# Performance work log

Hardware: AMD Instinct MI355X
Metric: run time of the kernel (lower is better)

Reference implementation:

```python
import jax, jax.numpy as jnp
import numpy as np

# config matching init_kwargs
J = 5
Q = 8
T = 15
C = 4
J_PHI = 2
B = 4
N = 65536

# near_sym_b level-1 lowpass (13-tap) from the dtcwt library; highpass via QMF modulation.
H0O = np.array([-0.00455690456024, -0.00543947593727, 0.01702522388155, 0.02382538479492,
                -0.10671180468666, 0.01186609203379, 0.56881042071212, 0.75614564389252,
                0.27529538466888, -0.11720388769911, -0.03887280126882, 0.03466034684485,
                -0.00388321199915], dtype=np.float32)
H1O = (((-1.0) ** np.arange(13)) * H0O[::-1]).astype(np.float32)
# qshift_a 10-tap filters for levels >= 2 (tree b = time-reversed tree a)
H0A = np.array([0.03516384, 0.0, -0.08832942, 0.23389032, 0.76027237,
                0.58751830, 0.0, -0.11430184, 0.0, 0.0], dtype=np.float32)
H0B = H0A[::-1].copy()
H1A = (((-1.0) ** np.arange(10)) * H0B).astype(np.float32)
H1B = H1A[::-1].copy()


def _dwconv(x, h, dilation):
    # depthwise 'same' conv; x: (B,C,N), h: (K,) fixed wavelet filter
    c = x.shape[1]
    k = h.shape[0]
    w = jnp.tile(jnp.asarray(h, x.dtype)[None, None, :], (c, 1, 1))
    tot = dilation * (k - 1)
    return jax.lax.conv_general_dilated(
        x, w, (1,), [(tot // 2, tot - tot // 2)], rhs_dilation=(dilation,),
        dimension_numbers=("NCH", "OIH", "NCH"), feature_group_count=c)


def _gconv(x, w, dilation):
    # grouped learnable conv: x (B,C,N), w (Q*C,1,T), groups=C, 'same' padding
    c = x.shape[1]
    t = w.shape[-1]
    tot = dilation * (t - 1)
    return jax.lax.conv_general_dilated(
        x, w, (1,), [(tot // 2, tot - tot // 2)], rhs_dilation=(dilation,),
        dimension_numbers=("NCH", "OIH", "NCH"), feature_group_count=c)


def _udtcwt(x):
    # undecimated dual-tree CWT (a-trous): returns lowpass and J (real, imag) bandpass pairs
    la, lb = x, x
    bps = []
    for j in range(J):
        d = 1 if j == 0 else 2 ** (j - 1)
        if j == 0:
            h0a, h1a, h0b, h1b = H0O, H1O, H0O, H1O
        else:
            h0a, h1a, h0b, h1b = H0A, H1A, H0B, H1B
        bps.append((_dwconv(la, h1a, d), _dwconv(lb, h1b, d)))
        la = _dwconv(la, h0a, d)
        lb = _dwconv(lb, h0b, d)
    return 0.5 * (la + lb), bps


def _downsample(x):
    # J_phi x (near_sym_b lowpass then ::2 decimation)
    for _ in range(J_PHI):
        x = _dwconv(x, H0O, 1)[:, :, ::2]
    return x


def _forward(x, conv_w, roots, beta):
    lp, bps = _udtcwt(x)
    outs = []
    for j in range(J):
        d = 1 if j == 0 else 2 ** (j - 1)
        scale = 2.0 ** (0.5 * j)  # sqrt(2)**j
        r = _gconv(bps[j][0], conv_w[j], d) / scale
        im = _gconv(bps[j][1], conv_w[j], d) / scale
        u = jnp.sqrt(r * r + im * im)  # ModulusStable
        alpha = jax.nn.sigmoid(roots[j])[None, :, None]  # (1, Q*C, 1)
        u = (jnp.maximum(u, -beta) + beta) ** alpha  # PowerStable
        outs.append(_downsample(u))
    return jnp.concatenate(outs, axis=1)  # (B, C*J*Q, N/2**J_phi)


def setup_inputs() -> dict:
    key = jax.random.key(0)
    kx, kw = jax.random.split(key)
    x = jax.random.normal(kx, (B, C, N), dtype=jnp.float32)
    bound = float(1.0 / np.sqrt(T))  # torch Conv1d default init (in/groups=1)
    conv_w = jax.random.uniform(kw, (J, Q * C, 1, T), dtype=jnp.float32, minval=-bound, maxval=bound)
    roots = jnp.ones((J, Q * C), dtype=jnp.float32)  # module inits root to ones
    beta = jnp.full((1,), 0.01, dtype=jnp.float32)
    return {"x": x, "conv_w": conv_w, "roots": roots, "beta": beta}


def reference(x, conv_w, roots, beta):
    return _forward(x, conv_w, roots, beta)
```

## Files before the change

### kernel.cpp

```cpp
#include <hip/hip_runtime.h>
#include <hip/hip_bf16.h>

typedef float v2f __attribute__((ext_vector_type(2)));

#define B_    4
#define C_    4
#define Q_    8
#define J_    5
#define T_    15
#define NSIG  65536
#define N2SIG 32768
#define NOUT  16384
#define NCH   (B_ * C_)

constexpr float H0Oc[13] = {
    -0.00455690456024f, -0.00543947593727f,  0.01702522388155f,  0.02382538479492f,
    -0.10671180468666f,  0.01186609203379f,  0.56881042071212f,  0.75614564389252f,
     0.27529538466888f, -0.11720388769911f, -0.03887280126882f,  0.03466034684485f,
    -0.00388321199915f };
constexpr float H1Oc[13] = {
    -0.00388321199915f, -0.03466034684485f, -0.03887280126882f,  0.11720388769911f,
     0.27529538466888f, -0.75614564389252f,  0.56881042071212f, -0.01186609203379f,
    -0.10671180468666f, -0.02382538479492f,  0.01702522388155f,  0.00543947593727f,
    -0.00455690456024f };
constexpr float H0Ac[10] = {
     0.03516384f, 0.0f, -0.08832942f, 0.23389032f, 0.76027237f,
     0.58751830f, 0.0f, -0.11430184f, 0.0f, 0.0f };
constexpr float H0Bc[10] = {
     0.0f, 0.0f, -0.11430184f, 0.0f, 0.58751830f,
     0.76027237f, 0.23389032f, -0.08832942f, 0.0f, 0.03516384f };
constexpr float H1Ac[10] = {
     0.0f, 0.0f, -0.11430184f, 0.0f, 0.58751830f,
    -0.76027237f, 0.23389032f, 0.08832942f, 0.0f, -0.03516384f };
constexpr float H1Bc[10] = {
    -0.03516384f, 0.0f, 0.08832942f, 0.23389032f, -0.76027237f,
     0.58751830f, 0.0f, -0.11430184f, 0.0f, 0.0f };

struct Gtab { float v[37]; };
constexpr Gtab make_g() {
    Gtab g{};
    for (int n = 0; n < 37; ++n) {
        float s = 0.f;
        for (int k = 0; k < 13; ++k) {
            int l = n - 2 * k;
            if (l >= 0 && l < 13) s += H0Oc[k] * H0Oc[l];
        }
        g.v[n] = s;
    }
    return g;
}
constexpr Gtab cG = make_g();

#define M2    256
#define NUcnt 1057
#define NUP   1064
#define NBcnt 1169
#define NBP   1176
#define S_    1320

#define SMEM_FLOATS (5280 + 2 * NBP)

__device__ __forceinline__ v2f zmask(v2f a, bool ok) {
    if (!ok) { a.x = 0.f; a.y = 0.f; }
    return a;
}

template<int D, bool EDGE>
__device__ __forceinline__ void post_stage(
        const v2f* __restrict__ sRI, v2f* __restrict__ U0, v2f* __restrict__ U1,
        const float* __restrict__ cw, const float* __restrict__ roots,
        float beta, int j, int b, int c, int m0, int mt, int tid,
        float* __restrict__ out) {
    const float lg_is = -0.5f * (float)j;
    const float beta2 = beta * exp2f(0.5f * (float)j);
    const int   u_lo  = 4 * m0 - 18;

    for (int g2 = 0; g2 < 2; ++g2) {
        float w[4][T_], al[4], cq[4];
        #pragma unroll
        for (int qq = 0; qq < 4; ++qq) {
            const int o = c * Q_ + g2 * 4 + qq;
            #pragma unroll
            for (int t = 0; t < T_; t++) w[qq][t] = cw[(size_t)(j * 32 + o) * T_ + t];
            al[qq] = 1.f / (1.f + __expf(-roots[j * 32 + o]));
            cq[qq] = al[qq] * lg_is;
        }

        for (int i = tid; i < NUcnt; i += 256) {
            const v2f* tp = sRI + (i + 56 - 7 * D);
            v2f taps[T_];
            #pragma unroll
            for (int t = 0; t < T_; t++) taps[t] = tp[t * D];
            bool ok = true;
            if constexpr (EDGE) {
                const int n = u_lo + i;
                ok = ((unsigned)n < (unsigned)NSIG);
            }
            float uq[4];
            #pragma unroll
            for (int qq = 0; qq < 4; ++qq) {
                v2f ri; ri.x = 0.f; ri.y = 0.f;
                #pragma unroll
                for (int t = 0; t < T_; t++) ri += w[qq][t] * taps[t];
                float z2 = fmaf(ri.x, ri.x, ri.y * ri.y);
                float us = __builtin_amdgcn_sqrtf(z2);
                float lg = __builtin_amdgcn_logf(us + beta2);
                float u  = __builtin_amdgcn_exp2f(fmaf(al[qq], lg, cq[qq]));
                if constexpr (EDGE) uq[qq] = ok ? u : 0.f;
                else                uq[qq] = u;
            }
            v2f p0; p0.x = uq[0]; p0.y = uq[1];
            v2f p1; p1.x = uq[2]; p1.y = uq[3];
            U0[i] = p0; U1[i] = p1;
        }
        __syncthreads();

        {
            const int m = m0 + tid;
            #pragma unroll
            for (int qp = 0; qp < 2; ++qp) {
                const v2f* up = qp ? U1 : U0;
                const v2f* ub = up + 4 * tid;
                v2f acc; acc.x = 0.f; acc.y = 0.f;
                #pragma unroll
                for (int n = 0; n < 37; ++n) acc += cG.v[n] * ub[n];
                if constexpr (EDGE) {
                    const bool edge = (mt == 0 && tid < 3) || (mt == 63 && tid >= 253);
                    if (edge) {
                        v2f a2; a2.x = 0.f; a2.y = 0.f;
                        for (int k = 0; k < 13; ++k) {
                            int p = 2 * m + k - 6;
                            if (p < 0 || p >= N2SIG) continue;
                            v2f v; v.x = 0.f; v.y = 0.f;
                            for (int l = 0; l < 13; ++l)
                                v += H0Oc[l] * up[4 * tid + 2 * k + l];
                            a2 += H0Oc[k] * v;
                        }
                        acc = a2;
                    }
                }
                const int o = c * Q_ + g2 * 4 + 2 * qp;
                out[((size_t)b * 160 + j * 32 + o)     * NOUT + m] = acc.x;
                out[((size_t)b * 160 + j * 32 + o + 1) * NOUT + m] = acc.y;
            }
        }
        __syncthreads();
    }
}

template<bool EDGE>
__device__ __forceinline__ void run_tile(
        float* __restrict__ smem,
        const float* __restrict__ x, const float* __restrict__ cw,
        const float* __restrict__ roots, float beta,
        float* __restrict__ out, int j, int mt, int ch, int tid) {
    float* X   = smem;
    float* L1  = smem + S_;
    v2f*   PP0 = (v2f*)smem;
    v2f*   PP1 = (v2f*)(smem + 2 * S_);
    v2f*   U0  = (v2f*)smem;
    v2f*   U1  = (v2f*)(smem + 2 * NUP);
    v2f*   sRI = (v2f*)(smem + 4 * S_);

    const int b   = ch >> 2, c = ch & 3;
    const int m0  = mt * M2;
    const int ofs = 4 * m0 - 147;
    const float* xc = x + (size_t)ch * NSIG;

    for (int p = tid; p < S_; p += 256) {
        if constexpr (EDGE) {
            int g = ofs + p;
            X[p] = ((unsigned)g < (unsigned)NSIG) ? xc[g] : 0.f;
        } else {
            X[p] = xc[ofs + p];
        }
    }
    __syncthreads();

    if (j == 0) {
        for (int i = tid; i < NBcnt; i += 256) {
            int p = 73 + i;
            float a = 0.f;
            #pragma unroll
            for (int k = 0; k < 13; k++) a += H1Oc[k] * X[p + k - 6];
            if constexpr (EDGE) { if ((unsigned)(ofs + p) >= (unsigned)NSIG) a = 0.f; }
            v2f r; r.x = a; r.y = a;
            sRI[i] = r;
        }
    } else {
        for (int p = 6 + tid; p < 1313; p += 256) {
            float a = 0.f;
            #pragma unroll
            for (int k = 0; k < 13; k++) a += H0Oc[k] * X[p + k - 6];
            if constexpr (EDGE) { if ((unsigned)(ofs + p) >= (unsigned)NSIG) a = 0.f; }
            L1[p] = a;
        }
        __syncthreads();
        if (j == 1) {
            for (int i = tid; i < NBcnt; i += 256) {
                int p = 73 + i;
                v2f r; r.x = 0.f; r.y = 0.f;
                #pragma unroll
                for (int k = 0; k < 10; k++) {
                    v2f hk; hk.x = H1Ac[k]; hk.y = H1Bc[k];
                    r += hk * L1[p + k - 4];
                }
                if constexpr (EDGE) r = zmask(r, (unsigned)(ofs + p) < (unsigned)NSIG);
                sRI[i] = r;
            }
        } else {
            for (int p = 10 + tid; p < 1308; p += 256) {
                v2f a; a.x = 0.f; a.y = 0.f;
                #pragma unroll
                for (int k = 0; k < 10; k++) {
                    v2f hk; hk.x = H0Ac[k]; hk.y = H0Bc[k];
                    a += hk * L1[p + k - 4];
                }
                if constexpr (EDGE) a = zmask(a, (unsigned)(ofs + p) < (unsigned)NSIG);
                PP1[p] = a;
            }
            __syncthreads();
            if (j == 2) {
                for (int i = tid; i < NBcnt; i += 256) {
                    int p = 73 + i;
                    v2f r; r.x = 0.f; r.y = 0.f;
                    #pragma unroll
                    for (int k = 0; k < 10; k++) {
                        v2f hk; hk.x = H1Ac[k]; hk.y = H1Bc[k];
                        r += hk * PP1[p + 2 * k - 9];
                    }
                    if constexpr (EDGE) r = zmask(r, (unsigned)(ofs + p) < (unsigned)NSIG);
                    sRI[i] = r;
                }
            } else {
                for (int p = 19 + tid; p < 1299; p += 256) {
                    v2f a; a.x = 0.f; a.y = 0.f;
                    #pragma unroll
                    for (int k = 0; k < 10; k++) {
                        v2f hk; hk.x = H0Ac[k]; hk.y = H0Bc[k];
                        a += hk * PP1[p + 2 * k - 9];
                    }
                    if constexpr (EDGE) a = zmask(a, (unsigned)(ofs + p) < (unsigned)NSIG);
                    PP0[p] = a;
                }
                __syncthreads();
                if (j == 3) {
                    for (int i = tid; i < NBcnt; i += 256) {
                        int p = 73 + i;
                        v2f r; r.x = 0.f; r.y = 0.f;
                        #pragma unroll
                        for (int k = 0; k < 10; k++) {
                            v2f hk; hk.x = H1Ac[k]; hk.y = H1Bc[k];
                            r += hk * PP0[p + 4 * k - 18];
                        }
                        if constexpr (EDGE) r = zmask(r, (unsigned)(ofs + p) < (unsigned)NSIG);
                        sRI[i] = r;
                    }
                } else {
                    for (int p = 37 + tid; p < 1281; p += 256) {
                        v2f a; a.x = 0.f; a.y = 0.f;
                        #pragma unroll
                        for (int k = 0; k < 10; k++) {
                            v2f hk; hk.x = H0Ac[k]; hk.y = H0Bc[k];
                            a += hk * PP0[p + 4 * k - 18];
                        }
                        if constexpr (EDGE) a = zmask(a, (unsigned)(ofs + p) < (unsigned)NSIG);
                        PP1[p] = a;
                    }
                    __syncthreads();
                    for (int i = tid; i < NBcnt; i += 256) {
                        int p = 73 + i;
                        v2f r; r.x = 0.f; r.y = 0.f;
                        #pragma unroll
                        for (int k = 0; k < 10; k++) {
                            v2f hk; hk.x = H1Ac[k]; hk.y = H1Bc[k];
                            r += hk * PP1[p + 8 * k - 36];
                        }
                        if constexpr (EDGE) r = zmask(r, (unsigned)(ofs + p) < (unsigned)NSIG);
                        sRI[i] = r;
                    }
                }
            }
        }
    }
    __syncthreads();

    float beta_ = beta;
    if (j == 0)      post_stage<1, EDGE>(sRI, U0, U1, cw, roots, beta_, 0, b, c, m0, mt, tid, out);
    else if (j == 1) post_stage<1, EDGE>(sRI, U0, U1, cw, roots, beta_, 1, b, c, m0, mt, tid, out);
    else if (j == 2) post_stage<2, EDGE>(sRI, U0, U1, cw, roots, beta_, 2, b, c, m0, mt, tid, out);
    else if (j == 3) post_stage<4, EDGE>(sRI, U0, U1, cw, roots, beta_, 3, b, c, m0, mt, tid, out);
    else             post_stage<8, EDGE>(sRI, U0, U1, cw, roots, beta_, 4, b, c, m0, mt, tid, out);
}

__global__ __launch_bounds__(256, 5) void murenn_all(
        const float* __restrict__ x,
        const float* __restrict__ cw,
        const float* __restrict__ roots,
        const float* __restrict__ beta_p,
        float* __restrict__ out) {
    __shared__ __align__(16) float smem[SMEM_FLOATS];
    const int tid = threadIdx.x;
    const int mt  = blockIdx.x;
    const int ch  = blockIdx.y;
    const int j   = blockIdx.z;
    const float beta = beta_p[0];

    if (mt == 0 || mt == 63)
        run_tile<true >(smem, x, cw, roots, beta, out, j, mt, ch, tid);
    else
        run_tile<false>(smem, x, cw, roots, beta, out, j, mt, ch, tid);
}

extern "C" void kernel_launch(void* const* d_in, const int* in_sizes, int n_in,
                              void* d_out, int out_size, void* d_ws, size_t ws_size,
                              hipStream_t stream) {
    (void)in_sizes; (void)n_in; (void)out_size; (void)d_ws; (void)ws_size;
    const float* x     = (const float*)d_in[0];
    const float* cw    = (const float*)d_in[1];
    const float* roots = (const float*)d_in[2];
    const float* beta  = (const float*)d_in[3];
    float* out = (float*)d_out;

    dim3 grid(NOUT / M2, NCH, J_);
    murenn_all<<<grid, 256, 0, stream>>>(x, cw, roots, beta, out);
}
```

Baseline: 162.3 us.

## Split fused kernel into shared wavelet-chain pass and per-level post pass via workspace

The fused kernel recomputed the whole undecimated DTCWT filter chain inside every (tile, channel, level) block, so the lower levels were recomputed up to five times. The change adds a chain kernel that computes all five bandpass planes once per tile and channel and writes them as interleaved real/imag pairs to the workspace. A second kernel then loads the plane for its level and runs the existing post stage. This trades the redundant compute for about 42 MB of global write plus read traffic and an extra launch, and it falls back to the fused kernel when no workspace is given.

New measurement: 167.5 us. +3.2%, slower.

```diff
diff --git a/kernel.cpp b/kernel.cpp
--- a/kernel.cpp
+++ b/kernel.cpp
@@ -58,7 +58,12 @@
 #define NBP   1176
 #define S_    1320
 
-#define SMEM_FLOATS (5280 + 2 * NBP)
+#define SMEM_ALL   (5280 + 2 * NBP)
+#define SMEM_CHAIN (4 * S_)
+#define SMEM_POST  (NBP + 2 * NUP)
+
+#define PLANE_V2F  ((size_t)J_ * NCH * NSIG)
+#define WS_BYTES   (PLANE_V2F * sizeof(v2f))
 
 __device__ __forceinline__ v2f zmask(v2f a, bool ok) {
     if (!ok) { a.x = 0.f; a.y = 0.f; }
@@ -145,6 +150,199 @@
             }
         }
         __syncthreads();
+    }
+}
+
+template<bool EDGE>
+__device__ __forceinline__ void chain_tile(
+        float* __restrict__ smem, const float* __restrict__ x,
+        v2f* __restrict__ bp, int mt, int ch, int tid) {
+    float* X   = smem;
+    float* L1  = smem + S_;
+    v2f*   PP0 = (v2f*)smem;
+    v2f*   PP1 = (v2f*)(smem + 2 * S_);
+
+    const int m0  = mt * M2;
+    const int ofs = 4 * m0 - 147;
+    const float* xc = x + (size_t)ch * NSIG;
+
+    for (int p = tid; p < S_; p += 256) {
+        if constexpr (EDGE) {
+            int g = ofs + p;
+            X[p] = ((unsigned)g < (unsigned)NSIG) ? xc[g] : 0.f;
+        } else {
+            X[p] = xc[ofs + p];
+        }
+    }
+    __syncthreads();
+
+    {
+        v2f* dst = bp + (size_t)(0 * NCH + ch) * NSIG + 4 * m0;
+        for (int idx = tid; idx < 1024; idx += 256) {
+            int p = 147 + idx;
+            float a = 0.f;
+            #pragma unroll
+            for (int k = 0; k < 13; k++) a += H1Oc[k] * X[p + k - 6];
+            v2f r; r.x = a; r.y = a;
+            dst[idx] = r;
+        }
+    }
+    for (int p = 6 + tid; p < 1313; p += 256) {
+        float a = 0.f;
+        #pragma unroll
+        for (int k = 0; k < 13; k++) a += H0Oc[k] * X[p + k - 6];
+        if constexpr (EDGE) { if ((unsigned)(ofs + p) >= (unsigned)NSIG) a = 0.f; }
+        L1[p] = a;
+    }
+    __syncthreads();
+
+    {
+        v2f* dst = bp + (size_t)(1 * NCH + ch) * NSIG + 4 * m0;
+        for (int idx = tid; idx < 1024; idx += 256) {
+            int p = 147 + idx;
+            v2f r; r.x = 0.f; r.y = 0.f;
+            #pragma unroll
+            for (int k = 0; k < 10; k++) {
+                v2f hk; hk.x = H1Ac[k]; hk.y = H1Bc[k];
+                r += hk * L1[p + k - 4];
+            }
+            dst[idx] = r;
+        }
+    }
+    for (int p = 10 + tid; p < 1308; p += 256) {
+        v2f a; a.x = 0.f; a.y = 0.f;
+        #pragma unroll
+        for (int k = 0; k < 10; k++) {
+            v2f hk; hk.x = H0Ac[k]; hk.y = H0Bc[k];
+            a += hk * L1[p + k - 4];
+        }
+        if constexpr (EDGE) a = zmask(a, (unsigned)(ofs + p) < (unsigned)NSIG);
+        PP1[p] = a;
+    }
+    __syncthreads();
+
+    {
+        v2f* dst = bp + (size_t)(2 * NCH + ch) * NSIG + 4 * m0;
+        for (int idx = tid; idx < 1024; idx += 256) {
+            int p = 147 + idx;
+            v2f r; r.x = 0.f; r.y = 0.f;
+            #pragma unroll
+            for (int k = 0; k < 10; k++) {
+                v2f hk; hk.x = H1Ac[k]; hk.y = H1Bc[k];
+                r += hk * PP1[p + 2 * k - 9];
+            }
+            dst[idx] = r;
+        }
+    }
+    for (int p = 19 + tid; p < 1299; p += 256) {
+        v2f a; a.x = 0.f; a.y = 0.f;
+        #pragma unroll
+        for (int k = 0; k < 10; k++) {
+            v2f hk; hk.x = H0Ac[k]; hk.y = H0Bc[k];
+            a += hk * PP1[p + 2 * k - 9];
+        }
+        if constexpr (EDGE) a = zmask(a, (unsigned)(ofs + p) < (unsigned)NSIG);
+        PP0[p] = a;
+    }
+    __syncthreads();
+
+    {
+        v2f* dst = bp + (size_t)(3 * NCH + ch) * NSIG + 4 * m0;
+        for (int idx = tid; idx < 1024; idx += 256) {
+            int p = 147 + idx;
+            v2f r; r.x = 0.f; r.y = 0.f;
+            #pragma unroll
+            for (int k = 0; k < 10; k++) {
+                v2f hk; hk.x = H1Ac[k]; hk.y = H1Bc[k];
+                r += hk * PP0[p + 4 * k - 18];
+            }
+            dst[idx] = r;
+        }
+    }
+    for (int p = 37 + tid; p < 1281; p += 256) {
+        v2f a; a.x = 0.f; a.y = 0.f;
+        #pragma unroll
+        for (int k = 0; k < 10; k++) {
+            v2f hk; hk.x = H0Ac[k]; hk.y = H0Bc[k];
+            a += hk * PP0[p + 4 * k - 18];
+        }
+        if constexpr (EDGE) a = zmask(a, (unsigned)(ofs + p) < (unsigned)NSIG);
+        PP1[p] = a;
+    }
+    __syncthreads();
+
+    {
+        v2f* dst = bp + (size_t)(4 * NCH + ch) * NSIG + 4 * m0;
+        for (int idx = tid; idx < 1024; idx += 256) {
+            int p = 147 + idx;
+            v2f r; r.x = 0.f; r.y = 0.f;
+            #pragma unroll
+            for (int k = 0; k < 10; k++) {
+                v2f hk; hk.x = H1Ac[k]; hk.y = H1Bc[k];
+                r += hk * PP1[p + 8 * k - 36];
+            }
+            dst[idx] = r;
+        }
+    }
+}
+
+__global__ __launch_bounds__(256, 5) void murenn_chain(
+        const float* __restrict__ x, v2f* __restrict__ bp) {
+    __shared__ __align__(16) float smem[SMEM_CHAIN];
+    const int tid = threadIdx.x;
+    const int mt  = blockIdx.x;
+    const int ch  = blockIdx.y;
+    if (mt == 0 || mt == 63) chain_tile<true >(smem, x, bp, mt, ch, tid);
+    else                     chain_tile<false>(smem, x, bp, mt, ch, tid);
+}
+
+__global__ __launch_bounds__(256, 6) void murenn_post(
+        const v2f* __restrict__ bp,
+        const float* __restrict__ cw,
+        const float* __restrict__ roots,
+        const float* __restrict__ beta_p,
+        float* __restrict__ out) {
+    __shared__ __align__(16) v2f smemv[SMEM_POST];
+    v2f* sRI = smemv;
+    v2f* U0  = smemv + NBP;
+    v2f* U1  = smemv + NBP + NUP;
+
+    const int tid = threadIdx.x;
+    const int mt  = blockIdx.x;
+    const int ch  = blockIdx.y;
+    const int j   = blockIdx.z;
+    const int b   = ch >> 2, c = ch & 3;
+    const int m0  = mt * M2;
+    const int base = 4 * m0 - 74;
+    const float beta = beta_p[0];
+    const v2f* plane = bp + (size_t)(j * NCH + ch) * NSIG;
+
+    const bool EDGE_T = (mt == 0 || mt == 63);
+    if (EDGE_T) {
+        for (int i = tid; i < NBcnt; i += 256) {
+            int n = base + i;
+            v2f v;
+            if ((unsigned)n < (unsigned)NSIG) v = plane[n];
+            else { v.x = 0.f; v.y = 0.f; }
+            sRI[i] = v;
+        }
+    } else {
+        for (int i = tid; i < NBcnt; i += 256) sRI[i] = plane[base + i];
+    }
+    __syncthreads();
+
+    if (EDGE_T) {
+        if (j == 0)      post_stage<1, true>(sRI, U0, U1, cw, roots, beta, 0, b, c, m0, mt, tid, out);
+        else if (j == 1) post_stage<1, true>(sRI, U0, U1, cw, roots, beta, 1, b, c, m0, mt, tid, out);
+        else if (j == 2) post_stage<2, true>(sRI, U0, U1, cw, roots, beta, 2, b, c, m0, mt, tid, out);
+        else if (j == 3) post_stage<4, true>(sRI, U0, U1, cw, roots, beta, 3, b, c, m0, mt, tid, out);
+        else             post_stage<8, true>(sRI, U0, U1, cw, roots, beta, 4, b, c, m0, mt, tid, out);
+    } else {
+        if (j == 0)      post_stage<1, false>(sRI, U0, U1, cw, roots, beta, 0, b, c, m0, mt, tid, out);
+        else if (j == 1) post_stage<1, false>(sRI, U0, U1, cw, roots, beta, 1, b, c, m0, mt, tid, out);
+        else if (j == 2) post_stage<2, false>(sRI, U0, U1, cw, roots, beta, 2, b, c, m0, mt, tid, out);
+        else if (j == 3) post_stage<4, false>(sRI, U0, U1, cw, roots, beta, 3, b, c, m0, mt, tid, out);
+        else             post_stage<8, false>(sRI, U0, U1, cw, roots, beta, 4, b, c, m0, mt, tid, out);
     }
 }
 
@@ -285,12 +483,11 @@
     }
     __syncthreads();
 
-    float beta_ = beta;
-    if (j == 0)      post_stage<1, EDGE>(sRI, U0, U1, cw, roots, beta_, 0, b, c, m0, mt, tid, out);
-    else if (j == 1) post_stage<1, EDGE>(sRI, U0, U1, cw, roots, beta_, 1, b, c, m0, mt, tid, out);
-    else if (j == 2) post_stage<2, EDGE>(sRI, U0, U1, cw, roots, beta_, 2, b, c, m0, mt, tid, out);
-    else if (j == 3) post_stage<4, EDGE>(sRI, U0, U1, cw, roots, beta_, 3, b, c, m0, mt, tid, out);
-    else             post_stage<8, EDGE>(sRI, U0, U1, cw, roots, beta_, 4, b, c, m0, mt, tid, out);
+    if (j == 0)      post_stage<1, EDGE>(sRI, U0, U1, cw, roots, beta, 0, b, c, m0, mt, tid, out);
+    else if (j == 1) post_stage<1, EDGE>(sRI, U0, U1, cw, roots, beta, 1, b, c, m0, mt, tid, out);
+    else if (j == 2) post_stage<2, EDGE>(sRI, U0, U1, cw, roots, beta, 2, b, c, m0, mt, tid, out);
+    else if (j == 3) post_stage<4, EDGE>(sRI, U0, U1, cw, roots, beta, 3, b, c, m0, mt, tid, out);
+    else             post_stage<8, EDGE>(sRI, U0, U1, cw, roots, beta, 4, b, c, m0, mt, tid, out);
 }
 
 __global__ __launch_bounds__(256, 5) void murenn_all(
@@ -299,13 +496,12 @@
         const float* __restrict__ roots,
         const float* __restrict__ beta_p,
         float* __restrict__ out) {
-    __shared__ __align__(16) float smem[SMEM_FLOATS];
+    __shared__ __align__(16) float smem[SMEM_ALL];
     const int tid = threadIdx.x;
     const int mt  = blockIdx.x;
     const int ch  = blockIdx.y;
     const int j   = blockIdx.z;
     const float beta = beta_p[0];
-
     if (mt == 0 || mt == 63)
         run_tile<true >(smem, x, cw, roots, beta, out, j, mt, ch, tid);
     else
@@ -315,13 +511,21 @@
 extern "C" void kernel_launch(void* const* d_in, const int* in_sizes, int n_in,
                               void* d_out, int out_size, void* d_ws, size_t ws_size,
                               hipStream_t stream) {
-    (void)in_sizes; (void)n_in; (void)out_size; (void)d_ws; (void)ws_size;
+    (void)in_sizes; (void)n_in; (void)out_size;
     const float* x     = (const float*)d_in[0];
     const float* cw    = (const float*)d_in[1];
     const float* roots = (const float*)d_in[2];
     const float* beta  = (const float*)d_in[3];
     float* out = (float*)d_out;
 
-    dim3 grid(NOUT / M2, NCH, J_);
-    murenn_all<<<grid, 256, 0, stream>>>(x, cw, roots, beta, out);
-}
+    if (d_ws != nullptr && ws_size >= WS_BYTES) {
+        v2f* bp = (v2f*)d_ws;
+        dim3 gA(NOUT / M2, NCH);
+        murenn_chain<<<gA, 256, 0, stream>>>(x, bp);
+        dim3 gB(NOUT / M2, NCH, J_);
+        murenn_post<<<gB, 256, 0, stream>>>(bp, cw, roots, beta, out);
+    } else {
+        dim3 grid(NOUT / M2, NCH, J_);
+        murenn_all<<<grid, 256, 0, stream>>>(x, cw, roots, beta, out);
+    }
+}
```
